# Kernel optimization log

Measured on AMD Instinct MI355X. Metric: run time of the kernel, lower is better.

Reference implementation:

```python
import jax, jax.numpy as jnp
import numpy as np

B, I, H = 8192, 1024, 1024


def setup_inputs() -> dict:
    key = jax.random.key(0)
    ks = jax.random.split(key, 11)
    s = 1.0 / np.sqrt(I + H)  # torch Linear default init scale
    return {
        "input": jax.random.normal(ks[0], (B, I), jnp.float32),
        "hidden_state": jax.random.normal(ks[1], (B, H), jnp.float32),
        "cell_state": jax.random.normal(ks[2], (B, H), jnp.float32),
        "W_f": jax.random.uniform(ks[3], (I + H, H), jnp.float32, -s, s),
        "b_f": jax.random.uniform(ks[4], (H,), jnp.float32, -s, s),
        "W_i": jax.random.uniform(ks[5], (I + H, H), jnp.float32, -s, s),
        "b_i": jax.random.uniform(ks[6], (H,), jnp.float32, -s, s),
        "W_c": jax.random.uniform(ks[7], (I + H, H), jnp.float32, -s, s),
        "b_c": jax.random.uniform(ks[8], (H,), jnp.float32, -s, s),
        "W_o": jax.random.uniform(ks[9], (I + H, H), jnp.float32, -s, s),
        "b_o": jax.random.uniform(ks[10], (H,), jnp.float32, -s, s),
    }


def reference(input, hidden_state, cell_state, W_f, b_f, W_i, b_i, W_c, b_c, W_o, b_o):
    # Classic LSTM cell (cell='LSTM' intended path):
    # combined = [x, h]; four gate GEMMs; fused elementwise gate combine.
    combined = jnp.concatenate([input, hidden_state], axis=1)  # [B, I+H]
    # One fused GEMM for all 4 gates (weights concatenated along output dim)
    W = jnp.concatenate([W_f, W_i, W_c, W_o], axis=1)          # [I+H, 4H]
    b = jnp.concatenate([b_f, b_i, b_c, b_o], axis=0)          # [4H]
    gates = combined @ W + b                                   # [B, 4H]
    f, i, c_dash, o = jnp.split(gates, 4, axis=1)
    f = jax.nn.sigmoid(f)
    i = jax.nn.sigmoid(i)
    o = jax.nn.sigmoid(o)
    new_cell = f * cell_state + i * jnp.tanh(c_dash)
    new_hidden = o * jnp.tanh(new_cell)
    return new_hidden, new_cell
```

## Files before the change

kernel.cpp:

```cpp
#include <hip/hip_runtime.h>
#include <hip/hip_bf16.h>
#include <cstdint>


#define BROWS 8192
#define IH    2048
#define HDIM  1024

typedef __bf16 bf16x8 __attribute__((ext_vector_type(8)));
typedef float  f32x4  __attribute__((ext_vector_type(4)));

__global__ void pack_A(const float* __restrict__ x, const float* __restrict__ hs,
                       __bf16* __restrict__ A) {
    size_t t = (size_t)blockIdx.x * 256 + threadIdx.x;
    size_t e = t * 8;
    int row = (int)(e >> 11);
    int col = (int)(e & 2047);
    const float* src = (col < 1024) ? (x + (size_t)row * 1024 + col)
                                    : (hs + (size_t)row * 1024 + (col - 1024));
    const float4 v0 = ((const float4*)src)[0];
    const float4 v1 = ((const float4*)src)[1];
    bf16x8 r;
    r[0] = (__bf16)v0.x; r[1] = (__bf16)v0.y; r[2] = (__bf16)v0.z; r[3] = (__bf16)v0.w;
    r[4] = (__bf16)v1.x; r[5] = (__bf16)v1.y; r[6] = (__bf16)v1.z; r[7] = (__bf16)v1.w;
    *(bf16x8*)(A + e) = r;
}

__global__ void pack_W(const float* __restrict__ Wf, const float* __restrict__ Wi,
                       const float* __restrict__ Wc, const float* __restrict__ Wo,
                       __bf16* __restrict__ Wt) {
    __shared__ float tile[32][33];
    const int g = blockIdx.z;
    const float* W = (g == 0) ? Wf : (g == 1) ? Wi : (g == 2) ? Wc : Wo;
    const int n0 = blockIdx.x * 32;
    const int k0 = blockIdx.y * 32;
    const int tx = threadIdx.x;
    const int ty = threadIdx.y;
#pragma unroll
    for (int i = 0; i < 4; ++i) {
        int k = k0 + ty + i * 8;
        tile[ty + i * 8][tx] = W[(size_t)k * HDIM + n0 + tx];
    }
    __syncthreads();
#pragma unroll
    for (int i = 0; i < 4; ++i) {
        int n = n0 + ty + i * 8;
        Wt[(size_t)(g * HDIM + n) * IH + k0 + tx] = (__bf16)tile[tx][ty + i * 8];
    }
}

#define BM 128
#define BH 32
#define BK 64

__global__ void lstm_gemm(const __bf16* __restrict__ A,
                          const __bf16* __restrict__ Wt,
                          const float* __restrict__ cell,
                          const float* __restrict__ bF_, const float* __restrict__ bI_,
                          const float* __restrict__ bC_, const float* __restrict__ bO_,
                          float* __restrict__ out)
{
    __shared__ __bf16 As[BM * BK];
    __shared__ __bf16 Bs[4 * BH * BK];

    const int tid  = threadIdx.x;
    const int wave = tid >> 6;
    const int lane = tid & 63;
    const int quad = lane >> 4;
    const int l16  = lane & 15;
    const int wr   = wave >> 1;
    const int wc   = wave & 1;

    const int m0 = blockIdx.y * BM;
    const int h0 = blockIdx.x * BH;

    const int lrow = lane >> 3;
    const int lk   = (lane & 7) * 8;

    f32x4 acc[4][4] = {};

    for (int k0 = 0; k0 < IH; k0 += BK) {
#pragma unroll
        for (int i = 0; i < 4; ++i) {
            int c = wave * 4 + i;
            int row = c * 8 + lrow;
            const __bf16* gp = A + (size_t)(m0 + row) * IH + k0 + lk;
            __bf16* lp = &As[c * 8 * BK];
            __builtin_amdgcn_global_load_lds(
                (const __attribute__((address_space(1))) unsigned*)gp,
                (__attribute__((address_space(3))) unsigned*)lp, 16, 0, 0);
        }
#pragma unroll
        for (int i = 0; i < 4; ++i) {
            int c = wave * 4 + i;
            int rl = c * 8 + lrow;
            int g = rl >> 5, hl = rl & 31;
            const __bf16* gp = Wt + (size_t)(g * HDIM + h0 + hl) * IH + k0 + lk;
            __bf16* lp = &Bs[c * 8 * BK];
            __builtin_amdgcn_global_load_lds(
                (const __attribute__((address_space(1))) unsigned*)gp,
                (__attribute__((address_space(3))) unsigned*)lp, 16, 0, 0);
        }
        __syncthreads();

#pragma unroll
        for (int ki = 0; ki < BK; ki += 32) {
            bf16x8 af[4], bg[4];
#pragma unroll
            for (int r = 0; r < 4; ++r)
                af[r] = *(const bf16x8*)&As[(wr * 64 + r * 16 + l16) * BK + ki + quad * 8];
#pragma unroll
            for (int g = 0; g < 4; ++g)
                bg[g] = *(const bf16x8*)&Bs[(g * 32 + wc * 16 + l16) * BK + ki + quad * 8];
#pragma unroll
            for (int g = 0; g < 4; ++g)
#pragma unroll
                for (int r = 0; r < 4; ++r)
                    acc[g][r] = __builtin_amdgcn_mfma_f32_16x16x32_bf16(
                        af[r], bg[g], acc[g][r], 0, 0, 0);
        }
        __syncthreads();
    }

    const int h = h0 + wc * 16 + l16;
    const float bF = bF_[h], bI = bI_[h], bC = bC_[h], bO = bO_[h];
#pragma unroll
    for (int r = 0; r < 4; ++r) {
#pragma unroll
        for (int reg = 0; reg < 4; ++reg) {
            const int m = m0 + wr * 64 + r * 16 + quad * 4 + reg;
            float pf = acc[0][r][reg] + bF;
            float pi = acc[1][r][reg] + bI;
            float pc = acc[2][r][reg] + bC;
            float po = acc[3][r][reg] + bO;
            float f  = 1.f / (1.f + __expf(-pf));
            float ig = 1.f / (1.f + __expf(-pi));
            float og = 1.f / (1.f + __expf(-po));
            float e2 = __expf(2.f * pc);
            float cd = (e2 - 1.f) / (e2 + 1.f);
            float cp = cell[(size_t)m * HDIM + h];
            float cn = f * cp + ig * cd;
            float ec = __expf(2.f * cn);
            float tc = (ec - 1.f) / (ec + 1.f);
            out[(size_t)m * HDIM + h] = og * tc;
            out[(size_t)BROWS * HDIM + (size_t)m * HDIM + h] = cn;
        }
    }
}

extern "C" void kernel_launch(void* const* d_in, const int* in_sizes, int n_in,
                              void* d_out, int out_size, void* d_ws, size_t ws_size,
                              hipStream_t stream) {
    const float* x  = (const float*)d_in[0];
    const float* hs = (const float*)d_in[1];
    const float* cs = (const float*)d_in[2];
    const float* Wf = (const float*)d_in[3];
    const float* bF = (const float*)d_in[4];
    const float* Wi = (const float*)d_in[5];
    const float* bI = (const float*)d_in[6];
    const float* Wc = (const float*)d_in[7];
    const float* bC = (const float*)d_in[8];
    const float* Wo = (const float*)d_in[9];
    const float* bO = (const float*)d_in[10];
    float* out = (float*)d_out;

    __bf16* A  = (__bf16*)d_ws;
    __bf16* Wt = (__bf16*)((char*)d_ws + (size_t)BROWS * IH * 2);

    pack_A<<<(BROWS * IH / 8) / 256, 256, 0, stream>>>(x, hs, A);
    pack_W<<<dim3(HDIM / 32, IH / 32, 4), dim3(32, 8), 0, stream>>>(Wf, Wi, Wc, Wo, Wt);
    lstm_gemm<<<dim3(HDIM / BH, BROWS / BM), 256, 0, stream>>>(A, Wt, cs, bF, bI, bC, bO, out);
}
```

Measured before the change: 330.6 us.

## Merge pack kernels into one launch and XOR-swizzle GEMM shared-memory tiles

```diff
diff --git a/kernel.cpp b/kernel.cpp
--- a/kernel.cpp
+++ b/kernel.cpp
@@ -10,42 +10,55 @@
 typedef __bf16 bf16x8 __attribute__((ext_vector_type(8)));
 typedef float  f32x4  __attribute__((ext_vector_type(4)));
 
-__global__ void pack_A(const float* __restrict__ x, const float* __restrict__ hs,
-                       __bf16* __restrict__ A) {
-    size_t t = (size_t)blockIdx.x * 256 + threadIdx.x;
-    size_t e = t * 8;
-    int row = (int)(e >> 11);
-    int col = (int)(e & 2047);
-    const float* src = (col < 1024) ? (x + (size_t)row * 1024 + col)
-                                    : (hs + (size_t)row * 1024 + (col - 1024));
-    const float4 v0 = ((const float4*)src)[0];
-    const float4 v1 = ((const float4*)src)[1];
-    bf16x8 r;
-    r[0] = (__bf16)v0.x; r[1] = (__bf16)v0.y; r[2] = (__bf16)v0.z; r[3] = (__bf16)v0.w;
-    r[4] = (__bf16)v1.x; r[5] = (__bf16)v1.y; r[6] = (__bf16)v1.z; r[7] = (__bf16)v1.w;
-    *(bf16x8*)(A + e) = r;
-}
-
-__global__ void pack_W(const float* __restrict__ Wf, const float* __restrict__ Wi,
-                       const float* __restrict__ Wc, const float* __restrict__ Wo,
-                       __bf16* __restrict__ Wt) {
-    __shared__ float tile[32][33];
-    const int g = blockIdx.z;
-    const float* W = (g == 0) ? Wf : (g == 1) ? Wi : (g == 2) ? Wc : Wo;
-    const int n0 = blockIdx.x * 32;
-    const int k0 = blockIdx.y * 32;
-    const int tx = threadIdx.x;
-    const int ty = threadIdx.y;
+__global__ void pack_fused(const float* __restrict__ x, const float* __restrict__ hs,
+                           const float* __restrict__ Wf, const float* __restrict__ Wi,
+                           const float* __restrict__ Wc, const float* __restrict__ Wo,
+                           __bf16* __restrict__ A, __bf16* __restrict__ Wt) {
+    __shared__ float tile[64][65];
+    const int bb = blockIdx.x;
+    if (bb < 4096) {
+        size_t t = (size_t)bb * 256 + threadIdx.x;
+        size_t e = t * 16;
+        int row = (int)(e >> 11);
+        int col = (int)(e & 2047);
+        const float* src = (col < 1024) ? (x + (size_t)row * 1024 + col)
+                                        : (hs + (size_t)row * 1024 + (col - 1024));
+        float4 v0 = ((const float4*)src)[0];
+        float4 v1 = ((const float4*)src)[1];
+        float4 v2 = ((const float4*)src)[2];
+        float4 v3 = ((const float4*)src)[3];
+        bf16x8 r0, r1;
+        r0[0]=(__bf16)v0.x; r0[1]=(__bf16)v0.y; r0[2]=(__bf16)v0.z; r0[3]=(__bf16)v0.w;
+        r0[4]=(__bf16)v1.x; r0[5]=(__bf16)v1.y; r0[6]=(__bf16)v1.z; r0[7]=(__bf16)v1.w;
+        r1[0]=(__bf16)v2.x; r1[1]=(__bf16)v2.y; r1[2]=(__bf16)v2.z; r1[3]=(__bf16)v2.w;
+        r1[4]=(__bf16)v3.x; r1[5]=(__bf16)v3.y; r1[6]=(__bf16)v3.z; r1[7]=(__bf16)v3.w;
+        *(bf16x8*)(A + e) = r0;
+        *(bf16x8*)(A + e + 8) = r1;
+    } else {
+        const int wb = bb - 4096;
+        const int g  = wb & 3;
+        const int rest = wb >> 2;
+        const int n0 = (rest & 15) * 64;
+        const int k0 = (rest >> 4) * 64;
+        const float* W = (g == 0) ? Wf : (g == 1) ? Wi : (g == 2) ? Wc : Wo;
+        const int tx = threadIdx.x & 63;
+        const int ty = threadIdx.x >> 6;
 #pragma unroll
-    for (int i = 0; i < 4; ++i) {
-        int k = k0 + ty + i * 8;
-        tile[ty + i * 8][tx] = W[(size_t)k * HDIM + n0 + tx];
-    }
-    __syncthreads();
+        for (int i = 0; i < 16; ++i) {
+            int k = ty + i * 4;
+            tile[k][tx] = W[(size_t)(k0 + k) * HDIM + n0 + tx];
+        }
+        __syncthreads();
+        const int n  = threadIdx.x >> 2;
+        const int kq = threadIdx.x & 3;
+        __bf16* dst = Wt + (size_t)(g * HDIM + n0 + n) * IH + k0 + kq * 16;
 #pragma unroll
-    for (int i = 0; i < 4; ++i) {
-        int n = n0 + ty + i * 8;
-        Wt[(size_t)(g * HDIM + n) * IH + k0 + tx] = (__bf16)tile[tx][ty + i * 8];
+        for (int s = 0; s < 2; ++s) {
+            bf16x8 r;
+#pragma unroll
+            for (int j = 0; j < 8; ++j) r[j] = (__bf16)tile[kq * 16 + s * 8 + j][n];
+            *(bf16x8*)(dst + s * 8) = r;
+        }
     }
 }
 
@@ -70,12 +83,13 @@
     const int l16  = lane & 15;
     const int wr   = wave >> 1;
     const int wc   = wave & 1;
+    const int sw   = l16 & 7;
 
     const int m0 = blockIdx.y * BM;
     const int h0 = blockIdx.x * BH;
 
     const int lrow = lane >> 3;
-    const int lk   = (lane & 7) * 8;
+    const int lk   = (((lane & 7) ^ (lrow & 7)) << 3);
 
     f32x4 acc[4][4] = {};
 
@@ -105,13 +119,19 @@
 
 #pragma unroll
         for (int ki = 0; ki < BK; ki += 32) {
+            const int kk = ki >> 3;
+            const int ch = (kk + quad) ^ sw;
             bf16x8 af[4], bg[4];
 #pragma unroll
-            for (int r = 0; r < 4; ++r)
-                af[r] = *(const bf16x8*)&As[(wr * 64 + r * 16 + l16) * BK + ki + quad * 8];
+            for (int r = 0; r < 4; ++r) {
+                int ra = wr * 64 + r * 16 + l16;
+                af[r] = *(const bf16x8*)&As[ra * BK + (ch << 3)];
+            }
 #pragma unroll
-            for (int g = 0; g < 4; ++g)
-                bg[g] = *(const bf16x8*)&Bs[(g * 32 + wc * 16 + l16) * BK + ki + quad * 8];
+            for (int g = 0; g < 4; ++g) {
+                int rb = g * 32 + wc * 16 + l16;
+                bg[g] = *(const bf16x8*)&Bs[rb * BK + (ch << 3)];
+            }
 #pragma unroll
             for (int g = 0; g < 4; ++g)
 #pragma unroll
@@ -167,7 +187,6 @@
     __bf16* A  = (__bf16*)d_ws;
     __bf16* Wt = (__bf16*)((char*)d_ws + (size_t)BROWS * IH * 2);
 
-    pack_A<<<(BROWS * IH / 8) / 256, 256, 0, stream>>>(x, hs, A);
-    pack_W<<<dim3(HDIM / 32, IH / 32, 4), dim3(32, 8), 0, stream>>>(Wf, Wi, Wc, Wo, Wt);
+    pack_fused<<<4096 + 2048, 256, 0, stream>>>(x, hs, Wf, Wi, Wc, Wo, A, Wt);
     lstm_gemm<<<dim3(HDIM / BH, BROWS / BM), 256, 0, stream>>>(A, Wt, cs, bF, bI, bC, bO, out);
 }
```

Result: faster. 317.7 us (-3.9%).

## XOR-swizzle LDS tiles in LSTM GEMM and vectorize the pack kernels

Applied to the files above, without the earlier changes.

```diff
diff --git a/kernel.cpp b/kernel.cpp
--- a/kernel.cpp
+++ b/kernel.cpp
@@ -7,45 +7,50 @@
 #define IH    2048
 #define HDIM  1024
 
+typedef __bf16 bf16x4 __attribute__((ext_vector_type(4)));
 typedef __bf16 bf16x8 __attribute__((ext_vector_type(8)));
 typedef float  f32x4  __attribute__((ext_vector_type(4)));
 
 __global__ void pack_A(const float* __restrict__ x, const float* __restrict__ hs,
                        __bf16* __restrict__ A) {
-    size_t t = (size_t)blockIdx.x * 256 + threadIdx.x;
-    size_t e = t * 8;
-    int row = (int)(e >> 11);
-    int col = (int)(e & 2047);
-    const float* src = (col < 1024) ? (x + (size_t)row * 1024 + col)
-                                    : (hs + (size_t)row * 1024 + (col - 1024));
-    const float4 v0 = ((const float4*)src)[0];
-    const float4 v1 = ((const float4*)src)[1];
-    bf16x8 r;
-    r[0] = (__bf16)v0.x; r[1] = (__bf16)v0.y; r[2] = (__bf16)v0.z; r[3] = (__bf16)v0.w;
-    r[4] = (__bf16)v1.x; r[5] = (__bf16)v1.y; r[6] = (__bf16)v1.z; r[7] = (__bf16)v1.w;
-    *(bf16x8*)(A + e) = r;
+    const int tid = threadIdx.x;
+    const size_t base = (size_t)blockIdx.x * 2048;
+#pragma unroll
+    for (int p = 0; p < 2; ++p) {
+        size_t e = base + (size_t)p * 1024 + (size_t)tid * 4;
+        int row = (int)(e >> 11);
+        int col = (int)(e & 2047);
+        const float* src = (col < 1024) ? (x + (size_t)row * 1024 + col)
+                                        : (hs + (size_t)row * 1024 + (col - 1024));
+        float4 v = *(const float4*)src;
+        bf16x4 r;
+        r[0] = (__bf16)v.x; r[1] = (__bf16)v.y; r[2] = (__bf16)v.z; r[3] = (__bf16)v.w;
+        *(bf16x4*)(A + e) = r;
+    }
 }
 
 __global__ void pack_W(const float* __restrict__ Wf, const float* __restrict__ Wi,
                        const float* __restrict__ Wc, const float* __restrict__ Wo,
                        __bf16* __restrict__ Wt) {
     __shared__ float tile[32][33];
-    const int g = blockIdx.z;
+    int b = blockIdx.x;
+    const int g = b & 3; b >>= 2;
+    const int nt = b & 31;
+    const int kt = b >> 5;
+    const int n0 = nt * 32, k0 = kt * 32;
     const float* W = (g == 0) ? Wf : (g == 1) ? Wi : (g == 2) ? Wc : Wo;
-    const int n0 = blockIdx.x * 32;
-    const int k0 = blockIdx.y * 32;
-    const int tx = threadIdx.x;
-    const int ty = threadIdx.y;
-#pragma unroll
-    for (int i = 0; i < 4; ++i) {
-        int k = k0 + ty + i * 8;
-        tile[ty + i * 8][tx] = W[(size_t)k * HDIM + n0 + tx];
+    const int tid = threadIdx.x;
+    {
+        const int k = tid >> 3, c = tid & 7;
+        *(float4*)&tile[k][c * 4] = *(const float4*)&W[(size_t)(k0 + k) * HDIM + n0 + c * 4];
     }
     __syncthreads();
+    {
+        const int n = tid >> 3, kq = tid & 7;
+        bf16x4 r;
 #pragma unroll
-    for (int i = 0; i < 4; ++i) {
-        int n = n0 + ty + i * 8;
-        Wt[(size_t)(g * HDIM + n) * IH + k0 + tx] = (__bf16)tile[tx][ty + i * 8];
+        for (int j = 0; j < 4; ++j) r[j] = (__bf16)tile[kq * 4 + j][n];
+        *(bf16x4*)&Wt[(size_t)(g * HDIM + n0 + n) * IH + k0 + kq * 4] = r;
     }
 }
 
@@ -70,12 +75,13 @@
     const int l16  = lane & 15;
     const int wr   = wave >> 1;
     const int wc   = wave & 1;
+    const int sw   = l16 & 7;
 
     const int m0 = blockIdx.y * BM;
     const int h0 = blockIdx.x * BH;
 
     const int lrow = lane >> 3;
-    const int lk   = (lane & 7) * 8;
+    const int lk   = (((lane & 7) ^ (lrow & 7)) << 3);
 
     f32x4 acc[4][4] = {};
 
@@ -105,13 +111,19 @@
 
 #pragma unroll
         for (int ki = 0; ki < BK; ki += 32) {
+            const int kk = ki >> 3;
+            const int ch = (kk + quad) ^ sw;
             bf16x8 af[4], bg[4];
 #pragma unroll
-            for (int r = 0; r < 4; ++r)
-                af[r] = *(const bf16x8*)&As[(wr * 64 + r * 16 + l16) * BK + ki + quad * 8];
+            for (int r = 0; r < 4; ++r) {
+                int ra = wr * 64 + r * 16 + l16;
+                af[r] = *(const bf16x8*)&As[ra * BK + (ch << 3)];
+            }
 #pragma unroll
-            for (int g = 0; g < 4; ++g)
-                bg[g] = *(const bf16x8*)&Bs[(g * 32 + wc * 16 + l16) * BK + ki + quad * 8];
+            for (int g = 0; g < 4; ++g) {
+                int rb = g * 32 + wc * 16 + l16;
+                bg[g] = *(const bf16x8*)&Bs[rb * BK + (ch << 3)];
+            }
 #pragma unroll
             for (int g = 0; g < 4; ++g)
 #pragma unroll
@@ -167,7 +179,7 @@
     __bf16* A  = (__bf16*)d_ws;
     __bf16* Wt = (__bf16*)((char*)d_ws + (size_t)BROWS * IH * 2);
 
-    pack_A<<<(BROWS * IH / 8) / 256, 256, 0, stream>>>(x, hs, A);
-    pack_W<<<dim3(HDIM / 32, IH / 32, 4), dim3(32, 8), 0, stream>>>(Wf, Wi, Wc, Wo, Wt);
+    pack_A<<<BROWS * IH / 2048, 256, 0, stream>>>(x, hs, A);
+    pack_W<<<4 * 32 * 64, 256, 0, stream>>>(Wf, Wi, Wc, Wo, Wt);
     lstm_gemm<<<dim3(HDIM / BH, BROWS / BM), 256, 0, stream>>>(A, Wt, cs, bF, bI, bC, bO, out);
 }
```

Measured after the change: 317.2 us. -4.1%, faster.
